# Performance work log

Measured on AMD Instinct MI355X. Metric: run time of the kernel, lower is better.

The kernel has to match this reference:

```python
import jax, jax.numpy as jnp
import numpy as np

B, L, H = 8, 512, 768
W = 5          # max_phrase_len
K = 32         # max_phrases
P = 256        # phrase_dim
EPS = 1e-5
NEG = -1e30


def layernorm(x, g, b):
    m = jnp.mean(x, axis=-1, keepdims=True)
    v = jnp.var(x, axis=-1, keepdims=True)
    return (x - m) * jax.lax.rsqrt(v + EPS) * g + b


def setup_inputs() -> dict:
    key = jax.random.key(0)
    ks = jax.random.split(key, 12)
    s = 0.02
    return {
        "hidden": jax.random.normal(ks[0], (B, L, H), dtype=jnp.float32),
        "attention_mask": jnp.ones((B, L), dtype=jnp.int32),
        # span_scorer: Linear(4H->H), LayerNorm(H), ReLU, Linear(H->1)
        "w1": jax.random.normal(ks[1], (4 * H, H), dtype=jnp.float32) * s,
        "b1": jnp.zeros((H,), dtype=jnp.float32),
        "g1": jnp.ones((H,), dtype=jnp.float32),
        "beta1": jnp.zeros((H,), dtype=jnp.float32),
        "w2": jax.random.normal(ks[2], (H, 1), dtype=jnp.float32) * s,
        "b2": jnp.zeros((1,), dtype=jnp.float32),
        # proj: Linear(H->P)
        "wp": jax.random.normal(ks[3], (H, P), dtype=jnp.float32) * s,
        "bp": jnp.zeros((P,), dtype=jnp.float32),
        # attention_gate: Linear(H->H/2), Tanh, Linear(H/2->1)
        "wg1": jax.random.normal(ks[4], (H, H // 2), dtype=jnp.float32) * s,
        "bg1": jnp.zeros((H // 2,), dtype=jnp.float32),
        "wg2": jax.random.normal(ks[5], (H // 2, 1), dtype=jnp.float32) * s,
        "bg2": jnp.zeros((1,), dtype=jnp.float32),
        # out_norm: LayerNorm(P)
        "gout": jnp.ones((P,), dtype=jnp.float32),
        "bout": jnp.zeros((P,), dtype=jnp.float32),
    }


def reference(hidden, attention_mask, w1, b1, g1, beta1, w2, b2,
              wp, bp, wg1, bg1, wg2, bg2, gout, bout):
    mask = attention_mask.astype(bool)  # [B,L]
    # validity of span (i, j=i+w): all tokens i..i+w in mask and i+w < L
    valids = []
    v = mask
    for w in range(W):
        if w > 0:
            shifted = jnp.pad(mask[:, w:], ((0, 0), (0, w)), constant_values=False)
            v = v & shifted
        valids.append(v)
    valid = jnp.stack(valids, axis=2)  # [B,L,W]

    # span means via prefix sums
    prefix = jnp.pad(jnp.cumsum(hidden, axis=1), ((0, 0), (1, 0), (0, 0)))  # [B,L+1,H]
    i_idx = jnp.arange(L)
    j_idx = jnp.minimum(i_idx[:, None] + jnp.arange(W)[None, :], L - 1)  # [L,W]

    start = hidden[:, :, None, :]                                  # [B,L,1,H]
    end = hidden[:, j_idx]                                         # [B,L,W,H]
    span_sum = prefix[:, j_idx + 1] - prefix[:, i_idx][:, :, None, :]
    mean = span_sum / (jnp.arange(W, dtype=hidden.dtype) + 1.0)[None, None, :, None]
    diff = end - start
    start_b = jnp.broadcast_to(start, end.shape)
    feat = jnp.concatenate([start_b, end, mean, diff], axis=-1)    # [B,L,W,4H]

    h = feat @ w1 + b1
    h = jax.nn.relu(layernorm(h, g1, beta1))                       # dropout is eval-mode identity
    score = (h @ w2 + b2)[..., 0]                                  # [B,L,W]
    score = jnp.where(valid, score, NEG)

    flat_scores = score.reshape(B, L * W)
    top_scores, top_idx = jax.lax.top_k(flat_scores, K)            # [B,K]
    phrase_masks = top_scores > NEG / 2

    mean_flat = mean.reshape(B, L * W, H)
    embs = jnp.take_along_axis(mean_flat, top_idx[..., None], axis=1)  # [B,K,H]
    embs = jnp.where(phrase_masks[..., None], embs, 0.0)               # zero-pad features
    phrase_scores = jnp.where(phrase_masks, top_scores, -10.0)

    ti = top_idx // W
    tw = top_idx % W
    spans = jnp.stack([ti, ti + tw], axis=-1)                      # [B,K,2]
    spans = jnp.where(phrase_masks[..., None], spans, 0)

    gate_logits = (jnp.tanh(embs @ wg1 + bg1) @ wg2 + bg2)[..., 0]  # [B,K]
    gate_logits = jnp.where(phrase_masks, gate_logits, -1e9)
    phrase_attention = jax.nn.softmax(gate_logits, axis=-1)

    phrase_embeds = layernorm(embs @ wp + bp, gout, bout)           # [B,K,P]
    return phrase_embeds, phrase_masks, phrase_attention, phrase_scores, spans
```

## Files before the change

### kernel.cpp

```cpp
#include <hip/hip_runtime.h>
#include <float.h>
#include <math.h>
#include <stdint.h>

#define B_   8
#define L_   512
#define H_   768
#define W_   5
#define K_   32
#define P_   256
#define EPS_ 1e-5f
#define NEG_ -1e30f

typedef _Float16 half8 __attribute__((ext_vector_type(8)));
typedef _Float16 half4v __attribute__((ext_vector_type(4)));
typedef float floatx4 __attribute__((ext_vector_type(4)));

static const size_t OFF_X   = 0;
static const size_t OFF_AH  = 9437184;
static const size_t OFF_AL  = 11010048;
static const size_t OFF_BH  = 12582912;
static const size_t OFF_BL  = 13467648;
static const size_t OFF_SC  = 14352384;
static const size_t OFF_TS  = 14372864;
static const size_t OFF_TI  = 14373120;
static const size_t OFF_GL  = 14373376;
static const size_t OFF_EMB = 14373632;
static const size_t OFF_Y   = 14570240;

#define A_SCALE 8.0f
#define B_SCALE 64.0f
#define INV_SCALE (1.0f / 512.0f)

__global__ __launch_bounds__(256) void prep_kernel(const float* __restrict__ hid,
                                                   const float* __restrict__ w1,
                                                   _Float16* __restrict__ ah,
                                                   _Float16* __restrict__ al,
                                                   _Float16* __restrict__ bh,
                                                   _Float16* __restrict__ bl) {
    __shared__ float ld[64][65];
    if (blockIdx.x < 3072) {
        int idx = (blockIdx.x * 256 + threadIdx.x) * 4;
        float4 x = *(const float4*)(hid + idx);
        float xs[4] = {x.x * A_SCALE, x.y * A_SCALE, x.z * A_SCALE, x.w * A_SCALE};
        half4v h, l;
#pragma unroll
        for (int i = 0; i < 4; ++i) {
            _Float16 hi = (_Float16)xs[i];
            h[i] = hi;
            l[i] = (_Float16)(xs[i] - (float)hi);
        }
        *(half4v*)(ah + idx) = h;
        *(half4v*)(al + idx) = l;
    } else {
        int bid = blockIdx.x - 3072;
        int n0 = (bid / 12) * 64;
        int k0 = (bid % 12) * 64;
        int t = threadIdx.x;
        int rsel = n0 / 768;
        int c0 = n0 - rsel * 768;
#pragma unroll 4
        for (int r = 0; r < 16; ++r) {
            int idx = r * 256 + t;
            int kk = idx >> 6, nn = idx & 63;
            int k = k0 + kk, c = c0 + nn;
            float v;
            if (rsel == 0)      v = w1[(size_t)k * 768 + c] - w1[(size_t)(2304 + k) * 768 + c];
            else if (rsel == 1) v = w1[(size_t)(768 + k) * 768 + c] + w1[(size_t)(2304 + k) * 768 + c];
            else                v = w1[(size_t)(1536 + k) * 768 + c];
            ld[kk][nn] = v * B_SCALE;
        }
        __syncthreads();
#pragma unroll 4
        for (int r = 0; r < 16; ++r) {
            int idx = r * 256 + t;
            int nn = idx >> 6, kk = idx & 63;
            float v = ld[kk][nn];
            _Float16 h = (_Float16)v;
            _Float16 lo = (_Float16)(v - (float)h);
            size_t o = (size_t)(n0 + nn) * 768 + k0 + kk;
            bh[o] = h;
            bl[o] = lo;
        }
    }
}

typedef const __attribute__((address_space(1))) void* gas_ptr;
typedef __attribute__((address_space(3))) void* las_ptr;
__device__ __forceinline__ void async_ld16(const _Float16* g, _Float16* l) {
    __builtin_amdgcn_global_load_lds((gas_ptr)g, (las_ptr)l, 16, 0, 0);
}

__global__ __launch_bounds__(256) void mfma_gemm_kernel(const _Float16* __restrict__ Ah,
                                                        const _Float16* __restrict__ Al,
                                                        const _Float16* __restrict__ Bh,
                                                        const _Float16* __restrict__ Bl,
                                                        float* __restrict__ C) {
    __shared__ _Float16 sAh[2 * 4096];
    __shared__ _Float16 sAl[2 * 4096];
    __shared__ _Float16 sBh[2 * 2048];
    __shared__ _Float16 sBl[2 * 2048];
    int tid = threadIdx.x;
    int lane = tid & 63;
    int wave = tid >> 6;
    int m0 = blockIdx.x * 128, n0 = blockIdx.y * 64;

    const _Float16* src = (wave == 0) ? Ah : (wave == 1) ? Al : (wave == 2) ? Bh : Bl;
    _Float16* dstb = (wave == 0) ? sAh : (wave == 1) ? sAl : (wave == 2) ? sBh : sBl;
    int psz  = (wave < 2) ? 4096 : 2048;
    int nch  = (wave < 2) ? 8 : 4;
    int row0 = (wave < 2) ? m0 : n0;
    int qg = (lane & 3) ^ ((lane >> 3) & 3);
    const _Float16* gp = src + (size_t)(row0 + (lane >> 2)) * 768 + qg * 8;

    int wr = wave >> 1, wc = wave & 1;
    int off_lane = (lane & 15) * 64 + (((lane >> 4) ^ ((lane >> 1) & 3)) * 16);
    floatx4 acc[4][2];
#pragma unroll
    for (int i = 0; i < 4; ++i)
#pragma unroll
        for (int j = 0; j < 2; ++j)
            acc[i][j] = (floatx4){0.f, 0.f, 0.f, 0.f};

#pragma unroll
    for (int c = 0; c < 8; ++c) {
        if (c < nch) async_ld16(gp + (size_t)c * 16 * 768, dstb + c * 512);
    }

    int parity = 0;
    for (int k0 = 0; k0 < 768; k0 += 32) {
        __syncthreads();
        if (k0 + 32 < 768) {
            _Float16* dst = dstb + (parity ^ 1) * psz;
            const _Float16* g = gp + k0 + 32;
#pragma unroll
            for (int c = 0; c < 8; ++c) {
                if (c < nch) async_ld16(g + (size_t)c * 16 * 768, dst + c * 512);
            }
        }

        const char* bAh = (const char*)sAh + parity * 8192 + wr * 4096 + off_lane;
        const char* bAl = (const char*)sAl + parity * 8192 + wr * 4096 + off_lane;
        const char* bBh = (const char*)sBh + parity * 4096 + wc * 2048 + off_lane;
        const char* bBl = (const char*)sBl + parity * 4096 + wc * 2048 + off_lane;
        half8 a_h[4], a_l[4], b_h[2], b_l[2];
#pragma unroll
        for (int i = 0; i < 4; ++i) {
            a_h[i] = *(const half8*)(bAh + i * 1024);
            a_l[i] = *(const half8*)(bAl + i * 1024);
        }
#pragma unroll
        for (int j = 0; j < 2; ++j) {
            b_h[j] = *(const half8*)(bBh + j * 1024);
            b_l[j] = *(const half8*)(bBl + j * 1024);
        }
#pragma unroll
        for (int i = 0; i < 4; ++i)
#pragma unroll
            for (int j = 0; j < 2; ++j) {
                acc[i][j] = __builtin_amdgcn_mfma_f32_16x16x32_f16(a_h[i], b_h[j], acc[i][j], 0, 0, 0);
                acc[i][j] = __builtin_amdgcn_mfma_f32_16x16x32_f16(a_h[i], b_l[j], acc[i][j], 0, 0, 0);
                acc[i][j] = __builtin_amdgcn_mfma_f32_16x16x32_f16(a_l[i], b_h[j], acc[i][j], 0, 0, 0);
            }
        parity ^= 1;
    }

    int colc = lane & 15, quad = lane >> 4;
#pragma unroll
    for (int i = 0; i < 4; ++i) {
#pragma unroll
        for (int r = 0; r < 4; ++r) {
            int row = m0 + wr * 64 + i * 16 + quad * 4 + r;
            float* Cp = C + (size_t)row * 2304 + n0 + wc * 32 + colc;
#pragma unroll
            for (int j = 0; j < 2; ++j)
                Cp[j * 16] = acc[i][j][r] * INV_SCALE;
        }
    }
}

__global__ __launch_bounds__(256) void score_kernel(const float* __restrict__ X,
                                                    const int* __restrict__ mask,
                                                    const float* __restrict__ b1,
                                                    const float* __restrict__ g1,
                                                    const float* __restrict__ beta1,
                                                    const float* __restrict__ w2,
                                                    const float* __restrict__ b2,
                                                    float* __restrict__ scores) {
    int wave = threadIdx.x >> 6;
    int lane = threadIdx.x & 63;
    int bi = blockIdx.x * 4 + wave;
    int b = bi >> 9, i = bi & 511;

    float4 a[3], b1c[3], g1c[3], btc[3], w2c[3], ss[3], e[3];
    const float4* Xrow = (const float4*)(X + (size_t)bi * 2304);
#pragma unroll
    for (int q = 0; q < 3; ++q) {
        int f = lane + q * 64;
        a[q]   = Xrow[f];
        b1c[q] = ((const float4*)b1)[f];
        g1c[q] = ((const float4*)g1)[f];
        btc[q] = ((const float4*)beta1)[f];
        w2c[q] = ((const float4*)w2)[f];
        ss[q]  = make_float4(0.f, 0.f, 0.f, 0.f);
    }
    float bias2 = b2[0];
    int jcur = i - 1;
    float sc_loc[W_];

    for (int w = 0; w < W_; ++w) {
        int j = min(i + w, 511);
        const float4* Xj = (const float4*)(X + (size_t)(b * 512 + j) * 2304);
        if (j > jcur) {
#pragma unroll
            for (int q = 0; q < 3; ++q) {
                int f = lane + q * 64;
                float4 cc = Xj[384 + f];
                ss[q].x += cc.x; ss[q].y += cc.y; ss[q].z += cc.z; ss[q].w += cc.w;
                e[q] = Xj[192 + f];
            }
            jcur = j;
        }
        float invw = 1.0f / (float)(w + 1);
        float4 h[3];
        float psum = 0.f;
#pragma unroll
        for (int q = 0; q < 3; ++q) {
            h[q].x = a[q].x + e[q].x + ss[q].x * invw + b1c[q].x;
            h[q].y = a[q].y + e[q].y + ss[q].y * invw + b1c[q].y;
            h[q].z = a[q].z + e[q].z + ss[q].z * invw + b1c[q].z;
            h[q].w = a[q].w + e[q].w + ss[q].w * invw + b1c[q].w;
            psum += h[q].x + h[q].y + h[q].z + h[q].w;
        }
#pragma unroll
        for (int m = 1; m < 64; m <<= 1) psum += __shfl_xor(psum, m, 64);
        float mean = psum * (1.f / 768.f);

        float pv = 0.f;
#pragma unroll
        for (int q = 0; q < 3; ++q) {
            float dx = h[q].x - mean, dy = h[q].y - mean, dz = h[q].z - mean, dw = h[q].w - mean;
            pv += dx * dx + dy * dy + dz * dz + dw * dw;
        }
#pragma unroll
        for (int m = 1; m < 64; m <<= 1) pv += __shfl_xor(pv, m, 64);
        float rstd = rsqrtf(pv * (1.f / 768.f) + EPS_);

        float pd = 0.f;
#pragma unroll
        for (int q = 0; q < 3; ++q) {
            float yx = fmaxf((h[q].x - mean) * rstd * g1c[q].x + btc[q].x, 0.f);
            float yy = fmaxf((h[q].y - mean) * rstd * g1c[q].y + btc[q].y, 0.f);
            float yz = fmaxf((h[q].z - mean) * rstd * g1c[q].z + btc[q].z, 0.f);
            float yw = fmaxf((h[q].w - mean) * rstd * g1c[q].w + btc[q].w, 0.f);
            pd += yx * w2c[q].x + yy * w2c[q].y + yz * w2c[q].z + yw * w2c[q].w;
        }
#pragma unroll
        for (int m = 1; m < 64; m <<= 1) pd += __shfl_xor(pd, m, 64);
        sc_loc[w] = pd + bias2;
    }

    if (lane < W_) {
        int w = lane;
        bool ok = (i + w) < 512;
        if (ok) {
            for (int t = 0; t <= w; ++t) ok = ok && (mask[b * 512 + i + t] != 0);
        }
        scores[b * 2560 + i * 5 + w] = ok ? sc_loc[w] : NEG_;
    }
}

__device__ __forceinline__ uint64_t shfl_xor_u64(uint64_t x, int m) {
    uint32_t lo = (uint32_t)x, hi = (uint32_t)(x >> 32);
    lo = (uint32_t)__shfl_xor((int)lo, m, 64);
    hi = (uint32_t)__shfl_xor((int)hi, m, 64);
    return ((uint64_t)hi << 32) | lo;
}

__global__ __launch_bounds__(256) void topk_kernel(const float* __restrict__ scores,
                                                   float* __restrict__ tops,
                                                   int* __restrict__ topi,
                                                   float* __restrict__ out_masks,
                                                   float* __restrict__ out_scores,
                                                   float* __restrict__ out_spans) {
    int b = blockIdx.x;
    int tid = threadIdx.x;
    int lane = tid & 63;
    int wv = tid >> 6;
    __shared__ uint64_t lists[256 * 9];
    __shared__ uint64_t wmax[4];
    __shared__ uint64_t gS;

    uint64_t v[10];
#pragma unroll
    for (int q = 0; q < 10; ++q) {
        int t = q * 256 + tid;
        float f = scores[b * 2560 + t];
        uint32_t bits = __float_as_uint(f);
        uint32_t mk = bits ^ ((bits & 0x80000000u) ? 0xFFFFFFFFu : 0x80000000u);
        v[q] = ((uint64_t)mk << 32) | (uint64_t)(0xFFFFFFFFu - (uint32_t)t);
    }
#pragma unroll
    for (int p = 0; p < 5; ++p) {
#pragma unroll
        for (int i = 0; i < 9; i += 2) {
            if (v[i] < v[i + 1]) { uint64_t t = v[i]; v[i] = v[i + 1]; v[i + 1] = t; }
        }
#pragma unroll
        for (int i = 1; i < 9; i += 2) {
            if (v[i] < v[i + 1]) { uint64_t t = v[i]; v[i] = v[i + 1]; v[i + 1] = t; }
        }
    }
#pragma unroll
    for (int j = 0; j < 9; ++j) lists[tid * 9 + j] = v[j + 1];
    uint64_t my = v[0];
    int h = 0;

    for (int k = 0; k < K_; ++k) {
        uint64_t m = my;
#pragma unroll
        for (int s = 1; s < 64; s <<= 1) {
            uint64_t o = shfl_xor_u64(m, s);
            if (o > m) m = o;
        }
        if (lane == 0) wmax[wv] = m;
        __syncthreads();
        if (tid == 0) {
            uint64_t g = wmax[0];
#pragma unroll
            for (int q = 1; q < 4; ++q) if (wmax[q] > g) g = wmax[q];
            gS = g;
            uint32_t mk = (uint32_t)(g >> 32);
            uint32_t bits = mk ^ ((mk & 0x80000000u) ? 0x80000000u : 0xFFFFFFFFu);
            float tv = __uint_as_float(bits);
            int tix = (int)(0xFFFFFFFFu - (uint32_t)(g & 0xFFFFFFFFu));
            tops[b * 32 + k] = tv;
            topi[b * 32 + k] = tix;
            bool mm = tv > (NEG_ * 0.5f);
            out_masks[b * 32 + k] = mm ? 1.0f : 0.0f;
            out_scores[b * 32 + k] = mm ? tv : -10.0f;
            int tI = tix / 5, tw = tix % 5;
            out_spans[(b * 32 + k) * 2 + 0] = mm ? (float)tI : 0.0f;
            out_spans[(b * 32 + k) * 2 + 1] = mm ? (float)(tI + tw) : 0.0f;
        }
        __syncthreads();
        uint64_t g = gS;
        if (my == g) {
            my = (h < 9) ? lists[tid * 9 + h] : 0ull;
            ++h;
        }
    }
}

__global__ __launch_bounds__(256) void gather_emb_kernel(const float* __restrict__ hidden,
                                                         const float* __restrict__ tops,
                                                         const int* __restrict__ topi,
                                                         float* __restrict__ Embs) {
    int bk = blockIdx.x;
    int b = bk >> 5;
    int tid = threadIdx.x;
    int idx = topi[bk];
    bool valid = tops[bk] > (NEG_ * 0.5f);
    int tI = idx / 5, tw = idx % 5;
    int jend = min(tI + tw, L_ - 1);
    float inv = 1.0f / (float)(tw + 1);
#pragma unroll
    for (int q = 0; q < 3; ++q) {
        int c = tid + q * 256;
        float s = 0.f;
        if (valid) {
            for (int l = tI; l <= jend; ++l) s += hidden[(size_t)(b * 512 + l) * 768 + c];
            s *= inv;
        }
        Embs[(size_t)bk * 768 + c] = s;
    }
}

__global__ __launch_bounds__(256) void phrase_gemm_kernel(const float* __restrict__ Embs,
                                                          const float* __restrict__ wg1,
                                                          const float* __restrict__ bg1,
                                                          const float* __restrict__ wp,
                                                          const float* __restrict__ bp,
                                                          float* __restrict__ Y) {
    __shared__ float As[32][34];
    __shared__ float Bs[32][64];
    int tid = threadIdx.x;
    int m0 = blockIdx.x * 32;
    int cn0 = blockIdx.y * 64;
    const float* Wp; const float* biasp; int ldw;
    if (cn0 < 384) { Wp = wg1 + cn0;        biasp = bg1 + cn0;        ldw = 384; }
    else           { Wp = wp + (cn0 - 384); biasp = bp + (cn0 - 384); ldw = 256; }

    int tx = tid & 15;
    int ty = tid >> 4;
    int ar = tid >> 3, akq = (tid & 7) * 4;
    int bk = tid >> 3, bcq = (tid & 7) * 8;
    float acc[2][4] = {};

    for (int k0 = 0; k0 < 768; k0 += 32) {
        float4 av  = *(const float4*)(Embs + (size_t)(m0 + ar) * 768 + k0 + akq);
        float4 bv0 = *(const float4*)(Wp + (size_t)(k0 + bk) * ldw + bcq);
        float4 bv1 = *(const float4*)(Wp + (size_t)(k0 + bk) * ldw + bcq + 4);
        __syncthreads();
        As[akq + 0][ar] = av.x;
        As[akq + 1][ar] = av.y;
        As[akq + 2][ar] = av.z;
        As[akq + 3][ar] = av.w;
        *(float4*)&Bs[bk][bcq]     = bv0;
        *(float4*)&Bs[bk][bcq + 4] = bv1;
        __syncthreads();
#pragma unroll
        for (int kk = 0; kk < 32; ++kk) {
            float2 a = *(const float2*)&As[kk][ty * 2];
            float4 b = *(const float4*)&Bs[kk][tx * 4];
            acc[0][0] += a.x * b.x; acc[0][1] += a.x * b.y; acc[0][2] += a.x * b.z; acc[0][3] += a.x * b.w;
            acc[1][0] += a.y * b.x; acc[1][1] += a.y * b.y; acc[1][2] += a.y * b.z; acc[1][3] += a.y * b.w;
        }
    }
#pragma unroll
    for (int i = 0; i < 2; ++i) {
        float* Yp = Y + (size_t)(m0 + ty * 2 + i) * 640 + cn0 + tx * 4;
        float4 o = make_float4(acc[i][0] + biasp[tx * 4 + 0], acc[i][1] + biasp[tx * 4 + 1],
                               acc[i][2] + biasp[tx * 4 + 2], acc[i][3] + biasp[tx * 4 + 3]);
        *(float4*)Yp = o;
    }
}

__global__ __launch_bounds__(256) void phrase_post_kernel(const float* __restrict__ Y,
                                                          const float* __restrict__ wg2,
                                                          const float* __restrict__ bg2,
                                                          const float* __restrict__ tops,
                                                          const float* __restrict__ gout,
                                                          const float* __restrict__ bout,
                                                          float* __restrict__ gate,
                                                          float* __restrict__ out_embeds) {
    int wv = threadIdx.x >> 6, lane = threadIdx.x & 63;
    int row = blockIdx.x * 4 + wv;
    const float* Yrow = Y + (size_t)row * 640;

    float s = 0.f;
#pragma unroll
    for (int q = 0; q < 6; ++q) {
        int c = lane + q * 64;
        s += tanhf(Yrow[c]) * wg2[c];
    }
#pragma unroll
    for (int m = 1; m < 64; m <<= 1) s += __shfl_xor(s, m, 64);
    if (lane == 0) {
        bool valid = tops[row] > (NEG_ * 0.5f);
        gate[row] = valid ? (s + bg2[0]) : -1e9f;
    }

    float4 p = *(const float4*)(Yrow + 384 + lane * 4);
    float sm = p.x + p.y + p.z + p.w;
#pragma unroll
    for (int m = 1; m < 64; m <<= 1) sm += __shfl_xor(sm, m, 64);
    float mean = sm * (1.f / 256.f);
    float dx = p.x - mean, dy = p.y - mean, dz = p.z - mean, dw = p.w - mean;
    float v = dx * dx + dy * dy + dz * dz + dw * dw;
#pragma unroll
    for (int m = 1; m < 64; m <<= 1) v += __shfl_xor(v, m, 64);
    float rstd = rsqrtf(v * (1.f / 256.f) + EPS_);
    int c = lane * 4;
    float4 o;
    o.x = dx * rstd * gout[c]     + bout[c];
    o.y = dy * rstd * gout[c + 1] + bout[c + 1];
    o.z = dz * rstd * gout[c + 2] + bout[c + 2];
    o.w = dw * rstd * gout[c + 3] + bout[c + 3];
    *(float4*)(out_embeds + (size_t)row * 256 + c) = o;
}

__global__ void attn_kernel(const float* __restrict__ gate, float* __restrict__ out_attn) {
    int b = threadIdx.x;
    if (b < 8) {
        float mx = -FLT_MAX;
        for (int k = 0; k < 32; ++k) mx = fmaxf(mx, gate[b * 32 + k]);
        float e[32];
        float s = 0.f;
        for (int k = 0; k < 32; ++k) { e[k] = expf(gate[b * 32 + k] - mx); s += e[k]; }
        float inv = 1.f / s;
        for (int k = 0; k < 32; ++k) out_attn[b * 32 + k] = e[k] * inv;
    }
}

extern "C" void kernel_launch(void* const* d_in, const int* in_sizes, int n_in,
                              void* d_out, int out_size, void* d_ws, size_t ws_size,
                              hipStream_t stream) {
    const float* hidden = (const float*)d_in[0];
    const int*   amask  = (const int*)d_in[1];
    const float* w1     = (const float*)d_in[2];
    const float* b1     = (const float*)d_in[3];
    const float* g1     = (const float*)d_in[4];
    const float* beta1  = (const float*)d_in[5];
    const float* w2     = (const float*)d_in[6];
    const float* b2     = (const float*)d_in[7];
    const float* wp     = (const float*)d_in[8];
    const float* bp     = (const float*)d_in[9];
    const float* wg1    = (const float*)d_in[10];
    const float* bg1    = (const float*)d_in[11];
    const float* wg2    = (const float*)d_in[12];
    const float* bg2    = (const float*)d_in[13];
    const float* gout   = (const float*)d_in[14];
    const float* bout   = (const float*)d_in[15];

    float* ws = (float*)d_ws;
    float*     X    = ws + OFF_X;
    _Float16*  ah   = (_Float16*)(ws + OFF_AH);
    _Float16*  al   = (_Float16*)(ws + OFF_AL);
    _Float16*  bh   = (_Float16*)(ws + OFF_BH);
    _Float16*  bl   = (_Float16*)(ws + OFF_BL);
    float*     sc   = ws + OFF_SC;
    float*     ts   = ws + OFF_TS;
    int*       ti   = (int*)(ws + OFF_TI);
    float*     gl   = ws + OFF_GL;
    float*     Embs = ws + OFF_EMB;
    float*     Y    = ws + OFF_Y;

    float* out = (float*)d_out;
    float* out_embeds = out;
    float* out_masks  = out + 65536;
    float* out_attn   = out + 65792;
    float* out_scores = out + 66048;
    float* out_spans  = out + 66304;

    prep_kernel<<<3504, 256, 0, stream>>>(hidden, w1, ah, al, bh, bl);
    mfma_gemm_kernel<<<dim3(32, 36), 256, 0, stream>>>(ah, al, bh, bl, X);
    score_kernel<<<1024, 256, 0, stream>>>(X, amask, b1, g1, beta1, w2, b2, sc);
    topk_kernel<<<8, 256, 0, stream>>>(sc, ts, ti, out_masks, out_scores, out_spans);
    gather_emb_kernel<<<256, 256, 0, stream>>>(hidden, ts, ti, Embs);
    phrase_gemm_kernel<<<dim3(8, 10), 256, 0, stream>>>(Embs, wg1, bg1, wp, bp, Y);
    phrase_post_kernel<<<64, 256, 0, stream>>>(Y, wg2, bg2, ts, gout, bout, gl, out_embeds);
    attn_kernel<<<1, 64, 0, stream>>>(gl, out_attn);
}
```

Baseline: 236.3 us.

## Prefetch next span row and fuse layernorm reductions in score kernel

The score kernel now loads the next row's end and cumulative-sum slices one iteration ahead (software pipelining) and fully unrolls the width loop. It computes mean and variance in a single pass with one combined shuffle reduction instead of two. It also replaces dynamic indexing of the per-lane score array with a select, so the array can stay in registers. The aim is to hide global-load latency and cut shuffle and reduction steps, at the cost of more registers and a single-pass variance that is less numerically robust.

```diff
diff --git a/kernel.cpp b/kernel.cpp
--- a/kernel.cpp
+++ b/kernel.cpp
@@ -192,12 +192,14 @@
     int bi = blockIdx.x * 4 + wave;
     int b = bi >> 9, i = bi & 511;
 
-    float4 a[3], b1c[3], g1c[3], btc[3], w2c[3], ss[3], e[3];
-    const float4* Xrow = (const float4*)(X + (size_t)bi * 2304);
+    const float4* base = (const float4*)(X + (size_t)(b * 512) * 2304);
+    float4 a[3], b1c[3], g1c[3], btc[3], w2c[3], ss[3], e_c[3], c_c[3], e_n[3], c_n[3];
 #pragma unroll
     for (int q = 0; q < 3; ++q) {
         int f = lane + q * 64;
-        a[q]   = Xrow[f];
+        e_c[q] = base[(size_t)i * 576 + 192 + f];
+        c_c[q] = base[(size_t)i * 576 + 384 + f];
+        a[q]   = base[(size_t)i * 576 + f];
         b1c[q] = ((const float4*)b1)[f];
         g1c[q] = ((const float4*)g1)[f];
         btc[q] = ((const float4*)beta1)[f];
@@ -208,43 +210,45 @@
     int jcur = i - 1;
     float sc_loc[W_];
 
+#pragma unroll
     for (int w = 0; w < W_; ++w) {
-        int j = min(i + w, 511);
-        const float4* Xj = (const float4*)(X + (size_t)(b * 512 + j) * 2304);
-        if (j > jcur) {
+        if (w < W_ - 1) {
+            int jn = min(i + w + 1, 511);
 #pragma unroll
             for (int q = 0; q < 3; ++q) {
                 int f = lane + q * 64;
-                float4 cc = Xj[384 + f];
-                ss[q].x += cc.x; ss[q].y += cc.y; ss[q].z += cc.z; ss[q].w += cc.w;
-                e[q] = Xj[192 + f];
+                e_n[q] = base[(size_t)jn * 576 + 192 + f];
+                c_n[q] = base[(size_t)jn * 576 + 384 + f];
+            }
+        }
+        int j = min(i + w, 511);
+        if (j > jcur) {
+#pragma unroll
+            for (int q = 0; q < 3; ++q) {
+                ss[q].x += c_c[q].x; ss[q].y += c_c[q].y; ss[q].z += c_c[q].z; ss[q].w += c_c[q].w;
             }
             jcur = j;
         }
         float invw = 1.0f / (float)(w + 1);
         float4 h[3];
-        float psum = 0.f;
+        float psum = 0.f, psq = 0.f;
 #pragma unroll
         for (int q = 0; q < 3; ++q) {
-            h[q].x = a[q].x + e[q].x + ss[q].x * invw + b1c[q].x;
-            h[q].y = a[q].y + e[q].y + ss[q].y * invw + b1c[q].y;
-            h[q].z = a[q].z + e[q].z + ss[q].z * invw + b1c[q].z;
-            h[q].w = a[q].w + e[q].w + ss[q].w * invw + b1c[q].w;
+            h[q].x = a[q].x + e_c[q].x + ss[q].x * invw + b1c[q].x;
+            h[q].y = a[q].y + e_c[q].y + ss[q].y * invw + b1c[q].y;
+            h[q].z = a[q].z + e_c[q].z + ss[q].z * invw + b1c[q].z;
+            h[q].w = a[q].w + e_c[q].w + ss[q].w * invw + b1c[q].w;
             psum += h[q].x + h[q].y + h[q].z + h[q].w;
-        }
-#pragma unroll
-        for (int m = 1; m < 64; m <<= 1) psum += __shfl_xor(psum, m, 64);
+            psq  += h[q].x * h[q].x + h[q].y * h[q].y + h[q].z * h[q].z + h[q].w * h[q].w;
+        }
+#pragma unroll
+        for (int m = 1; m < 64; m <<= 1) {
+            psum += __shfl_xor(psum, m, 64);
+            psq  += __shfl_xor(psq, m, 64);
+        }
         float mean = psum * (1.f / 768.f);
-
-        float pv = 0.f;
-#pragma unroll
-        for (int q = 0; q < 3; ++q) {
-            float dx = h[q].x - mean, dy = h[q].y - mean, dz = h[q].z - mean, dw = h[q].w - mean;
-            pv += dx * dx + dy * dy + dz * dz + dw * dw;
-        }
-#pragma unroll
-        for (int m = 1; m < 64; m <<= 1) pv += __shfl_xor(pv, m, 64);
-        float rstd = rsqrtf(pv * (1.f / 768.f) + EPS_);
+        float var  = psq * (1.f / 768.f) - mean * mean;
+        float rstd = rsqrtf(var + EPS_);
 
         float pd = 0.f;
 #pragma unroll
@@ -258,15 +262,24 @@
 #pragma unroll
         for (int m = 1; m < 64; m <<= 1) pd += __shfl_xor(pd, m, 64);
         sc_loc[w] = pd + bias2;
-    }
-
+
+        if (w < W_ - 1) {
+#pragma unroll
+            for (int q = 0; q < 3; ++q) { e_c[q] = e_n[q]; c_c[q] = c_n[q]; }
+        }
+    }
+
+    float outv = 0.f;
+#pragma unroll
+    for (int w = 0; w < W_; ++w)
+        if (lane == w) outv = sc_loc[w];
     if (lane < W_) {
         int w = lane;
         bool ok = (i + w) < 512;
         if (ok) {
             for (int t = 0; t <= w; ++t) ok = ok && (mask[b * 512 + i + t] != 0);
         }
-        scores[b * 2560 + i * 5 + w] = ok ? sc_loc[w] : NEG_;
+        scores[b * 2560 + i * 5 + w] = ok ? outv : NEG_;
     }
 }
 
```

New measurement: 233.4 us. No clear change (-1.2%).
